# Performance work log

Hardware: AMD Instinct MI355X
Metric: run time of the kernel (lower is better)

The kernel has to match this reference:

```python
import jax, jax.numpy as jnp
import numpy as np


def _lap(cost):
    """Jonker-Volgenant / e-maxx O(n^3) Hungarian (min-cost) on a square
    float64 cost matrix. Returns col index assigned to each row, matching
    scipy.optimize.linear_sum_assignment for square inputs.
    Inner column scan is vectorized with numpy.
    """
    n = cost.shape[0]
    INF = np.inf
    C = np.zeros((n + 1, n + 1), dtype=np.float64)
    C[1:, 1:] = cost  # 1-indexed
    u = np.zeros(n + 1)
    v = np.zeros(n + 1)
    p = np.zeros(n + 1, dtype=np.int64)    # p[j] = row matched to col j
    way = np.zeros(n + 1, dtype=np.int64)
    for i in range(1, n + 1):
        p[0] = i
        j0 = 0
        minv = np.full(n + 1, INF)
        used = np.zeros(n + 1, dtype=bool)
        while True:
            used[j0] = True
            i0 = p[j0]
            free = ~used
            free[0] = False
            cur = C[i0] - u[i0] - v
            upd = free & (cur < minv)
            minv = np.where(upd, cur, minv)
            way[upd] = j0
            mv = np.where(free, minv, INF)
            j1 = int(np.argmin(mv))
            delta = mv[j1]
            u[p[used]] += delta
            v[used] -= delta
            minv = np.where(free, minv - delta, minv)
            j0 = j1
            if p[j0] == 0:
                break
        # augment along alternating path
        while j0 != 0:
            j1 = way[j0]
            p[j0] = p[j1]
            j0 = j1
    col_for_row = np.zeros(n, dtype=np.int64)
    col_for_row[p[1:] - 1] = np.arange(n)
    return col_for_row


def _match(D_np):
    """Per-sample min-max normalize (detached) then Hungarian match."""
    B, N, _ = D_np.shape
    cols = np.zeros((B, N), dtype=np.int64)
    for b in range(B):
        Db = D_np[b]
        d_min = Db.min()
        d_range = Db.max() - d_min + 1e-8
        cols[b] = _lap((Db - d_min) / d_range)
    return cols


def setup_inputs() -> dict:
    key = jax.random.key(0)
    B, N = 32, 512
    D = jax.random.uniform(key, (B, N, N), dtype=jnp.float32)
    return {"D": D}


def reference(D):
    B, N, _ = D.shape
    # Matching indices are computed on detached, normalized costs (CPU, like
    # the original .cpu().numpy() round-trip).
    D_np = np.asarray(jax.device_get(D), dtype=np.float64)
    cols = jnp.asarray(_match(D_np))                      # [B, N]
    bi = jnp.arange(B)[:, None]
    ri = jnp.arange(N)[None, :]
    matched = D[bi, ri, cols]                             # [B, N], original D
    return matched.mean(axis=1).mean()
```

## Files before the change

kernel.cpp:

```cpp
#include <hip/hip_runtime.h>
#include <hip/hip_fp16.h>


#define NN 512
#define LPT 8
#define BIGF 1e30f
#define QCAP 2080
#define ARRCAP 1536
#define TOTAL_BLOCKS 256

typedef float v2f __attribute__((ext_vector_type(2)));
#define EL(a, s) ((a)[(s) >> 1][(s) & 1])

#define DPP_MINF(x, CTRL) do {                                                  \
    float _t = __int_as_float(__builtin_amdgcn_update_dpp(                      \
        __float_as_int(x), __float_as_int(x), CTRL, 0xf, 0xf, false));          \
    (x) = _t < (x) ? _t : (x);                                                  \
} while (0)

__device__ __forceinline__ float wave_min_f32(float x) {
    DPP_MINF(x, 0x111);
    DPP_MINF(x, 0x112);
    DPP_MINF(x, 0x114);
    DPP_MINF(x, 0x118);
    DPP_MINF(x, 0x142);
    DPP_MINF(x, 0x143);
    return __int_as_float(__builtin_amdgcn_readlane(__float_as_int(x), 63));
}

__device__ __forceinline__ void wavebar() { __builtin_amdgcn_wave_barrier(); }

__device__ __forceinline__ int sel8i(const int a[LPT], int slot) {
    int r = a[0];
    #pragma unroll
    for (int s = 1; s < LPT; ++s) r = (slot == s) ? a[s] : r;
    return r;
}
__device__ __forceinline__ float sel8fv(const v2f a[4], int slot) {
    float r = a[0][0];
    r = (slot == 1) ? a[0][1] : r;
    r = (slot == 2) ? a[1][0] : r;
    r = (slot == 3) ? a[1][1] : r;
    r = (slot == 4) ? a[2][0] : r;
    r = (slot == 5) ? a[2][1] : r;
    r = (slot == 6) ? a[3][0] : r;
    r = (slot == 7) ? a[3][1] : r;
    return r;
}
__device__ __forceinline__ void argmin8v(const v2f e2[4], float& bv, int& bs) {
    const float e0 = e2[0][0], e1 = e2[0][1], e2_ = e2[1][0], e3 = e2[1][1];
    const float e4 = e2[2][0], e5 = e2[2][1], e6 = e2[3][0], e7 = e2[3][1];
    float v01 = e1 < e0 ? e1 : e0;   int s01 = e1 < e0 ? 1 : 0;
    float v23 = e3 < e2_ ? e3 : e2_; int s23 = e3 < e2_ ? 3 : 2;
    float v45 = e5 < e4 ? e5 : e4;   int s45 = e5 < e4 ? 5 : 4;
    float v67 = e7 < e6 ? e7 : e6;   int s67 = e7 < e6 ? 7 : 6;
    float v03 = v23 < v01 ? v23 : v01; int s03 = v23 < v01 ? s23 : s01;
    float v47 = v67 < v45 ? v67 : v45; int s47 = v67 < v45 ? s67 : s45;
    bv = v47 < v03 ? v47 : v03;        bs = v47 < v03 ? s47 : s03;
}

__global__ void zero_kernel(int* __restrict__ done) {
    if (threadIdx.x == 0) *done = 0;
}

template <bool F16>
__global__ __launch_bounds__(64)
void hungarian_kernel(const float* __restrict__ D, const __half* __restrict__ Hm,
                      double* __restrict__ bsum, int* __restrict__ done, int B) {
    const int b    = blockIdx.x;
    const int lane = threadIdx.x;

    if (b >= B) {
        const unsigned long long t0 = __builtin_amdgcn_s_memrealtime();
        float x = 1.0f + (float)lane * 1e-6f;
        while (true) {
            #pragma unroll
            for (int k = 0; k < 512; ++k) x = __builtin_fmaf(x, 1.0000001f, 1e-9f);
            if (__hip_atomic_load(done, __ATOMIC_RELAXED, __HIP_MEMORY_SCOPE_AGENT) >= B)
                break;
            if (__builtin_amdgcn_s_memrealtime() - t0 > 1200000ull)
                break;
        }
        if (x == -1.0f) bsum[B] = (double)x;
        return;
    }

    const float*  __restrict__ Db = D + (size_t)b * NN * NN;
    const __half* __restrict__ Hb = F16 ? (Hm + (size_t)b * NN * NN) : (const __half*)nullptr;

    __shared__ __align__(16) int xrowc[NN];
    __shared__ __align__(16) int q[QCAP];

    for (int k = lane; k < NN; k += 64) xrowc[k] = 0;
    wavebar();

    const int col0 = lane * LPT;

    auto loadrow = [&](int r, v2f rv[4]) {
        if constexpr (F16) {
            const uint4 qv = *(const uint4*)(Hb + (size_t)(r - 1) * NN + col0);
            __half2 h0 = *(__half2*)&qv.x, h1 = *(__half2*)&qv.y,
                    h2 = *(__half2*)&qv.z, h3 = *(__half2*)&qv.w;
            float2 f0 = __half22float2(h0), f1 = __half22float2(h1),
                   f2 = __half22float2(h2), f3 = __half22float2(h3);
            v2f t0 = {f0.x, f0.y}, t1 = {f1.x, f1.y}, t2 = {f2.x, f2.y}, t3 = {f3.x, f3.y};
            rv[0] = t0; rv[1] = t1; rv[2] = t2; rv[3] = t3;
        } else {
            const float4* rp = (const float4*)(Db + (size_t)(r - 1) * NN + col0);
            const float4 a = rp[0], c = rp[1];
            v2f t0 = {a.x, a.y}, t1 = {a.z, a.w}, t2 = {c.x, c.y}, t3 = {c.z, c.w};
            rv[0] = t0; rv[1] = t1; rv[2] = t2; rv[3] = t3;
        }
    };
    auto loadsc = [&](int r, int j) -> float {
        if constexpr (F16) return __half2float(Hb[(size_t)(r - 1) * NN + (j - 1)]);
        else               return Db[(size_t)(r - 1) * NN + (j - 1)];
    };

    v2f   vv[4];
    int   preg[LPT];
    int   xr[LPT];

    auto build_queue = [&]() -> int {
        int cnt = 0;
        #pragma unroll
        for (int s = 0; s < LPT; ++s) cnt += (xr[s] == 0) ? 1 : 0;
        int pre = cnt;
        #pragma unroll
        for (int d = 1; d < 64; d <<= 1) {
            const int t = __shfl_up(pre, d, 64);
            if (lane >= d) pre += t;
        }
        const int total = __builtin_amdgcn_readlane(pre, 63);
        int ofs = pre - cnt;
        #pragma unroll
        for (int s = 0; s < LPT; ++s)
            if (xr[s] == 0) { q[ofs] = col0 + s + 1; ++ofs; }
        wavebar();
        return total;
    };

    {
        float cmin[LPT]; int cidx[LPT];
        #pragma unroll
        for (int s = 0; s < LPT; ++s) { cmin[s] = BIGF; cidx[s] = 0; }
        #pragma unroll 4
        for (int r = 1; r <= NN; ++r) {
            v2f rvx[4]; loadrow(r, rvx);
            #pragma unroll
            for (int s = 0; s < LPT; ++s) {
                const float x = EL(rvx, s);
                const bool c = x < cmin[s];
                cidx[s] = c ? r : cidx[s];
                cmin[s] = c ? x : cmin[s];
            }
        }
        #pragma unroll
        for (int s = 0; s < LPT; ++s) EL(vv, s) = cmin[s];
        #pragma unroll
        for (int s = 0; s < LPT; ++s) atomicMax(&xrowc[cidx[s] - 1], col0 + s + 1);
        wavebar();
        #pragma unroll
        for (int s = 0; s < LPT; ++s)
            preg[s] = (xrowc[cidx[s] - 1] == col0 + s + 1) ? cidx[s] : 0;
        const int4 x0 = *(const int4*)&xrowc[col0];
        const int4 x1 = *(const int4*)&xrowc[col0 + 4];
        xr[0]=x0.x; xr[1]=x0.y; xr[2]=x0.z; xr[3]=x0.w;
        xr[4]=x1.x; xr[5]=x1.y; xr[6]=x1.z; xr[7]=x1.w;
    }
    wavebar();

    {
        auto readjx = [&](int i) -> int {
            return __builtin_amdgcn_readlane(sel8i(xr, (i - 1) & 7), (i - 1) >> 3);
        };
        int jxN = readjx(1);
        v2f rvN[4];
        if (jxN) loadrow(1, rvN);
        for (int i = 1; i <= NN; ++i) {
            const int jx = jxN;
            v2f rcur[4];
            #pragma unroll
            for (int k = 0; k < 4; ++k) rcur[k] = rvN[k];
            jxN = (i < NN) ? readjx(i + 1) : 0;
            if (jxN) loadrow(i + 1, rvN);
            if (jx == 0) continue;
            const int  ow = (jx - 1) >> 3, sl = (jx - 1) & 7;
            const bool am = (lane == ow);
            v2f d2[4];
            #pragma unroll
            for (int k = 0; k < 4; ++k) d2[k] = rcur[k] - vv[k];
            float lm = BIGF;
            #pragma unroll
            for (int s = 0; s < LPT; ++s) {
                const float t = (am && s == sl) ? BIGF : EL(d2, s);
                lm = t < lm ? t : lm;
            }
            const float mu = wave_min_f32(lm);
            #pragma unroll
            for (int s = 0; s < LPT; ++s)
                if (am && s == sl) EL(vv, s) = EL(rcur, s) - mu;
        }
    }

    {
        int tail = build_queue();
        int head = 0, processed = 0;
        int iCur = 0;
        v2f rvC[4];
        if (tail > 0) { iCur = q[0]; loadrow(iCur, rvC); }
        while (head < tail && processed < ARRCAP) {
            const int i = iCur; ++head; ++processed;
            v2f rvA[4];
            #pragma unroll
            for (int k = 0; k < 4; ++k) rvA[k] = rvC[k];
            int iNxt = (head < tail) ? q[head] : 0;
            if (iNxt) loadrow(iNxt, rvC);

            v2f cur[4];
            #pragma unroll
            for (int k = 0; k < 4; ++k) cur[k] = rvA[k] - vv[k];
            float b1; int bs1; argmin8v(cur, b1, bs1);
            const int i1c = sel8i(preg, bs1);
            const float u1 = wave_min_f32(b1);
            const unsigned long long m1 = __ballot(b1 == u1);
            const int owner = __ffsll(m1) - 1;
            const int j1    = __builtin_amdgcn_readlane(col0 + bs1 + 1, owner);
            const int i1    = __builtin_amdgcn_readlane(i1c, owner);
            const bool am   = (lane == owner);
            #pragma unroll
            for (int s = 0; s < LPT; ++s)
                if (am && s == bs1) EL(cur, s) = BIGF;
            float b2 = BIGF;
            #pragma unroll
            for (int s = 0; s < LPT; ++s) { const float t = EL(cur, s); b2 = t < b2 ? t : b2; }
            const float u2 = wave_min_f32(b2);
            const bool steal  = (u1 < u2);
            const bool assign = (i1 == 0) || (steal && (tail < QCAP - 1));
            if (assign) {
                #pragma unroll
                for (int s = 0; s < LPT; ++s) {
                    if (am && s == bs1) {
                        if (steal) EL(vv, s) -= (u2 - u1);
                        preg[s] = i;
                    }
                }
                if (lane == 0) {
                    xrowc[i - 1] = j1;
                    if (i1) { xrowc[i1 - 1] = 0; q[tail] = i1; }
                }
                if (i1) {
                    if (!iNxt) { iNxt = i1; loadrow(iNxt, rvC); }
                    ++tail;
                }
            }
            iCur = iNxt;
            wavebar();
        }
    }
    wavebar();

    {
        const int4 x0 = *(const int4*)&xrowc[col0];
        const int4 x1 = *(const int4*)&xrowc[col0 + 4];
        xr[0]=x0.x; xr[1]=x0.y; xr[2]=x0.z; xr[3]=x0.w;
        xr[4]=x1.x; xr[5]=x1.y; xr[6]=x1.z; xr[7]=x1.w;
    }
    const int nfree = build_queue();

    int rootNext = (nfree > 0) ? q[0] : 0;
    v2f rv[4];
    if (rootNext) loadrow(rootNext, rv);
    for (int fi = 0; fi < nfree; ++fi) {
        const int rootI = rootNext;
        rootNext = (fi + 1 < nfree) ? q[fi + 1] : 0;

        v2f minv2[4], blk2[4], w2[4];
        int wayreg[LPT];
        #pragma unroll
        for (int k = 0; k < 4; ++k) {
            v2f big = {BIGF, BIGF}, zero = {0.0f, 0.0f};
            minv2[k] = big; blk2[k] = zero;
        }
        #pragma unroll
        for (int s = 0; s < LPT; ++s) wayreg[s] = 0;
        float uu = 0.0f;
        int   j0 = 0;

        #pragma unroll
        for (int k = 0; k < 4; ++k) w2[k] = rv[k] - vv[k];

        int j1 = 0; float dmin = 0.0f;
        while (true) {
            const v2f uu2 = {uu, uu};
            v2f e2[4];
            #pragma unroll
            for (int k = 0; k < 4; ++k) {
                const v2f c2 = (w2[k] - uu2) + blk2[k];
                const float c0 = c2[0], c1 = c2[1];
                const bool u0 = c0 < minv2[k][0];
                const bool u1 = c1 < minv2[k][1];
                wayreg[2*k]   = u0 ? j0 : wayreg[2*k];
                wayreg[2*k+1] = u1 ? j0 : wayreg[2*k+1];
                v2f m = minv2[k];
                m[0] = u0 ? c0 : m[0];
                m[1] = u1 ? c1 : m[1];
                minv2[k] = m;
                e2[k] = m + blk2[k];
            }
            float bv; int bs; argmin8v(e2, bv, bs);
            const int   i0c = sel8i(preg, bs);
            const float vjc = sel8fv(vv, bs);
            dmin = wave_min_f32(bv);
            const unsigned long long mk = __ballot(bv == dmin);
            const int owner = __ffsll(mk) - 1;
            j1 = __builtin_amdgcn_readlane(col0 + bs + 1, owner);
            const int i0n = __builtin_amdgcn_readlane(i0c, owner);
            if (i0n == 0) break;

            const float csc = loadsc(i0n, j1);
            loadrow(i0n, rv);
            const float vj1 = __int_as_float(__builtin_amdgcn_readlane(
                __float_as_int(vjc), owner));
            const bool am = (lane == owner);
            #pragma unroll
            for (int s = 0; s < LPT; ++s)
                if (am && s == bs) EL(blk2, s) = BIGF;

            uu = csc - vj1 - dmin;
            #pragma unroll
            for (int k = 0; k < 4; ++k) w2[k] = rv[k] - vv[k];
            j0 = j1;
        }
        const float dfinal = dmin;
        j0 = j1;

        if (rootNext) loadrow(rootNext, rv);

        #pragma unroll
        for (int s = 0; s < LPT; ++s)
            if (EL(blk2, s) == BIGF) EL(vv, s) += EL(minv2, s) - dfinal;

        int jj = j0;
        while (jj != 0) {
            const int sl = (jj - 1) & 7, ln = (jj - 1) >> 3;
            const int jp = __builtin_amdgcn_readlane(sel8i(wayreg, sl), ln);
            int nr;
            if (jp != 0) {
                const int sp = (jp - 1) & 7, lp = (jp - 1) >> 3;
                nr = __builtin_amdgcn_readlane(sel8i(preg, sp), lp);
            } else {
                nr = rootI;
            }
            #pragma unroll
            for (int s = 0; s < LPT; ++s)
                if (lane == ln && s == sl) preg[s] = nr;
            jj = jp;
        }
    }

    double acc = 0.0;
    #pragma unroll
    for (int s = 0; s < LPT; ++s) {
        const int r = preg[s];
        acc += (double)Db[(size_t)(r - 1) * NN + (col0 + s)];
    }
    #pragma unroll
    for (int m = 1; m < 64; m <<= 1) acc += __shfl_xor(acc, m, 64);
    if (lane == 0) {
        bsum[b] = acc;
        __threadfence();
        atomicAdd(done, 1);
    }
}

__global__ void finalize_kernel(const double* __restrict__ bsum, float* __restrict__ out, int B) {
    if (threadIdx.x == 0 && blockIdx.x == 0) {
        double acc = 0.0;
        for (int b = 0; b < B; ++b) acc += bsum[b] / (double)NN;
        out[0] = (float)(acc / (double)B);
    }
}

extern "C" void kernel_launch(void* const* d_in, const int* in_sizes, int n_in,
                              void* d_out, int out_size, void* d_ws, size_t ws_size,
                              hipStream_t stream) {
    (void)n_in; (void)out_size; (void)ws_size;
    const float* D    = (const float*)d_in[0];
    float*       out  = (float*)d_out;
    int*         done = (int*)d_ws;
    double*      bsum = (double*)((char*)d_ws + 64);

    const int B = in_sizes[0] / (NN * NN);

    zero_kernel<<<1, 64, 0, stream>>>(done);
    hungarian_kernel<false><<<dim3(TOTAL_BLOCKS), dim3(64), 0, stream>>>(D, nullptr, bsum, done, B);
    finalize_kernel<<<1, 64, 0, stream>>>(bsum, out, B);
}
```

Measured before the change: 2.493 ms.

## Speculatively prefetch next Dijkstra row using argmin over existing minv before scan

Restructures the inner shortest-augmenting-path loop so that, after each step, the wave computes the argmin over the current minv (excluding used columns). It then issues the row and scalar load for that candidate column one iteration early. When a wave ballot shows no newly relaxed column beats that speculative minimum, the prefetched row is used directly, hiding global-load latency behind the relaxation work. This costs an extra wave-wide reduction per step plus a second row buffer in registers, and wastes loads when the speculation misses. The unused F16 template path is also removed.

```diff
diff --git a/kernel.cpp b/kernel.cpp
--- a/kernel.cpp
+++ b/kernel.cpp
@@ -63,9 +63,8 @@
     if (threadIdx.x == 0) *done = 0;
 }
 
-template <bool F16>
 __global__ __launch_bounds__(64)
-void hungarian_kernel(const float* __restrict__ D, const __half* __restrict__ Hm,
+void hungarian_kernel(const float* __restrict__ D,
                       double* __restrict__ bsum, int* __restrict__ done, int B) {
     const int b    = blockIdx.x;
     const int lane = threadIdx.x;
@@ -85,8 +84,7 @@
         return;
     }
 
-    const float*  __restrict__ Db = D + (size_t)b * NN * NN;
-    const __half* __restrict__ Hb = F16 ? (Hm + (size_t)b * NN * NN) : (const __half*)nullptr;
+    const float* __restrict__ Db = D + (size_t)b * NN * NN;
 
     __shared__ __align__(16) int xrowc[NN];
     __shared__ __align__(16) int q[QCAP];
@@ -97,24 +95,13 @@
     const int col0 = lane * LPT;
 
     auto loadrow = [&](int r, v2f rv[4]) {
-        if constexpr (F16) {
-            const uint4 qv = *(const uint4*)(Hb + (size_t)(r - 1) * NN + col0);
-            __half2 h0 = *(__half2*)&qv.x, h1 = *(__half2*)&qv.y,
-                    h2 = *(__half2*)&qv.z, h3 = *(__half2*)&qv.w;
-            float2 f0 = __half22float2(h0), f1 = __half22float2(h1),
-                   f2 = __half22float2(h2), f3 = __half22float2(h3);
-            v2f t0 = {f0.x, f0.y}, t1 = {f1.x, f1.y}, t2 = {f2.x, f2.y}, t3 = {f3.x, f3.y};
-            rv[0] = t0; rv[1] = t1; rv[2] = t2; rv[3] = t3;
-        } else {
-            const float4* rp = (const float4*)(Db + (size_t)(r - 1) * NN + col0);
-            const float4 a = rp[0], c = rp[1];
-            v2f t0 = {a.x, a.y}, t1 = {a.z, a.w}, t2 = {c.x, c.y}, t3 = {c.z, c.w};
-            rv[0] = t0; rv[1] = t1; rv[2] = t2; rv[3] = t3;
-        }
+        const float4* rp = (const float4*)(Db + (size_t)(r - 1) * NN + col0);
+        const float4 a = rp[0], c = rp[1];
+        v2f t0 = {a.x, a.y}, t1 = {a.z, a.w}, t2 = {c.x, c.y}, t3 = {c.z, c.w};
+        rv[0] = t0; rv[1] = t1; rv[2] = t2; rv[3] = t3;
     };
     auto loadsc = [&](int r, int j) -> float {
-        if constexpr (F16) return __half2float(Hb[(size_t)(r - 1) * NN + (j - 1)]);
-        else               return Db[(size_t)(r - 1) * NN + (j - 1)];
+        return Db[(size_t)(r - 1) * NN + (j - 1)];
     };
 
     v2f   vv[4];
@@ -269,13 +256,14 @@
     const int nfree = build_queue();
 
     int rootNext = (nfree > 0) ? q[0] : 0;
-    v2f rv[4];
-    if (rootNext) loadrow(rootNext, rv);
+    v2f rvR[4], rvP[4];
+    float cscR = 0.0f, cscP = 0.0f;
+    if (rootNext) loadrow(rootNext, rvR);
     for (int fi = 0; fi < nfree; ++fi) {
         const int rootI = rootNext;
         rootNext = (fi + 1 < nfree) ? q[fi + 1] : 0;
 
-        v2f minv2[4], blk2[4], w2[4];
+        v2f minv2[4], blk2[4];
         int wayreg[LPT];
         #pragma unroll
         for (int k = 0; k < 4; ++k) {
@@ -284,58 +272,105 @@
         }
         #pragma unroll
         for (int s = 0; s < LPT; ++s) wayreg[s] = 0;
-        float uu = 0.0f;
+
         int   j0 = 0;
-
-        #pragma unroll
-        for (int k = 0; k < 4; ++k) w2[k] = rv[k] - vv[k];
+        float Me = BIGF; int j1E = 0, i0E = 0; float vjE = 0.0f;
+        float vjW = 0.0f, dminPrev = 0.0f;
+        bool  useSpec = false;
+        cscR = 0.0f;
 
         int j1 = 0; float dmin = 0.0f;
         while (true) {
+            v2f rvU[4]; float cscU;
+            if (useSpec) {
+                #pragma unroll
+                for (int k = 0; k < 4; ++k) rvU[k] = rvP[k];
+                cscU = cscP;
+            } else {
+                #pragma unroll
+                for (int k = 0; k < 4; ++k) rvU[k] = rvR[k];
+                cscU = cscR;
+            }
+            if (i0E != 0) {
+                cscP = loadsc(i0E, j1E);
+                loadrow(i0E, rvP);
+            }
+            const float uu = cscU - vjW - dminPrev;
             const v2f uu2 = {uu, uu};
-            v2f e2[4];
+            v2f c2[4], cs[4];
             #pragma unroll
             for (int k = 0; k < 4; ++k) {
-                const v2f c2 = (w2[k] - uu2) + blk2[k];
-                const float c0 = c2[0], c1 = c2[1];
-                const bool u0 = c0 < minv2[k][0];
-                const bool u1 = c1 < minv2[k][1];
+                const v2f w2 = rvU[k] - vv[k];
+                c2[k] = (w2 - uu2) + blk2[k];
+                cs[k] = c2[k] + blk2[k];
+            }
+            float bv_c; int bs_c; argmin8v(cs, bv_c, bs_c);
+            const int   i0cC = sel8i(preg, bs_c);
+            const float vjcC = sel8fv(vv, bs_c);
+            #pragma unroll
+            for (int k = 0; k < 4; ++k) {
+                const bool u0 = c2[k][0] < minv2[k][0];
+                const bool u1 = c2[k][1] < minv2[k][1];
                 wayreg[2*k]   = u0 ? j0 : wayreg[2*k];
                 wayreg[2*k+1] = u1 ? j0 : wayreg[2*k+1];
                 v2f m = minv2[k];
-                m[0] = u0 ? c0 : m[0];
-                m[1] = u1 ? c1 : m[1];
+                m[0] = u0 ? c2[k][0] : m[0];
+                m[1] = u1 ? c2[k][1] : m[1];
                 minv2[k] = m;
-                e2[k] = m + blk2[k];
-            }
-            float bv; int bs; argmin8v(e2, bv, bs);
-            const int   i0c = sel8i(preg, bs);
-            const float vjc = sel8fv(vv, bs);
-            dmin = wave_min_f32(bv);
-            const unsigned long long mk = __ballot(bv == dmin);
-            const int owner = __ffsll(mk) - 1;
-            j1 = __builtin_amdgcn_readlane(col0 + bs + 1, owner);
-            const int i0n = __builtin_amdgcn_readlane(i0c, owner);
+            }
+            int i0n;
+            const unsigned long long tst = __ballot(bv_c <= Me);
+            if (tst == 0ull) {
+                j1 = j1E; i0n = i0E; vjW = vjE; dmin = Me;
+                useSpec = true;
+            } else {
+                const float Mc = wave_min_f32(bv_c);
+                const unsigned long long mkc = __ballot(bv_c == Mc);
+                const int ownerC = __ffsll(mkc) - 1;
+                const int j1C = __builtin_amdgcn_readlane(col0 + bs_c + 1, ownerC);
+                const int i0C = __builtin_amdgcn_readlane(i0cC, ownerC);
+                const float vjC = __int_as_float(__builtin_amdgcn_readlane(
+                    __float_as_int(vjcC), ownerC));
+                dmin = Mc;
+                if (Mc == Me && j1E < j1C) {
+                    j1 = j1E; i0n = i0E; vjW = vjE; useSpec = true;
+                } else {
+                    j1 = j1C; i0n = i0C; vjW = vjC; useSpec = false;
+                }
+            }
             if (i0n == 0) break;
-
-            const float csc = loadsc(i0n, j1);
-            loadrow(i0n, rv);
-            const float vj1 = __int_as_float(__builtin_amdgcn_readlane(
-                __float_as_int(vjc), owner));
-            const bool am = (lane == owner);
-            #pragma unroll
-            for (int s = 0; s < LPT; ++s)
-                if (am && s == bs) EL(blk2, s) = BIGF;
-
-            uu = csc - vj1 - dmin;
-            #pragma unroll
-            for (int k = 0; k < 4; ++k) w2[k] = rv[k] - vv[k];
-            j0 = j1;
+            if (!useSpec) {
+                cscR = loadsc(i0n, j1);
+                loadrow(i0n, rvR);
+            }
+            {
+                const int ow = (j1 - 1) >> 3, sl = (j1 - 1) & 7;
+                const bool am = (lane == ow);
+                #pragma unroll
+                for (int s = 0; s < LPT; ++s)
+                    if (am && s == sl) EL(blk2, s) = BIGF;
+            }
+            j0 = j1; dminPrev = dmin;
+            {
+                v2f es[4];
+                #pragma unroll
+                for (int k = 0; k < 4; ++k) es[k] = minv2[k] + blk2[k];
+                float bv_e; int bs_e; argmin8v(es, bv_e, bs_e);
+                const int   i0cE = sel8i(preg, bs_e);
+                const float vjcE = sel8fv(vv, bs_e);
+                Me = wave_min_f32(bv_e);
+                const unsigned long long mke = __ballot(bv_e == Me);
+                const int ownerE = __ffsll(mke) - 1;
+                j1E = __builtin_amdgcn_readlane(col0 + bs_e + 1, ownerE);
+                i0E = __builtin_amdgcn_readlane(i0cE, ownerE);
+                vjE = __int_as_float(__builtin_amdgcn_readlane(
+                    __float_as_int(vjcE), ownerE));
+            }
         }
         const float dfinal = dmin;
         j0 = j1;
 
-        if (rootNext) loadrow(rootNext, rv);
+        if (rootNext) { cscR = 0.0f; loadrow(rootNext, rvR); }
 
         #pragma unroll
         for (int s = 0; s < LPT; ++s)
@@ -394,6 +429,6 @@
     const int B = in_sizes[0] / (NN * NN);
 
     zero_kernel<<<1, 64, 0, stream>>>(done);
-    hungarian_kernel<false><<<dim3(TOTAL_BLOCKS), dim3(64), 0, stream>>>(D, nullptr, bsum, done, B);
+    hungarian_kernel<<<dim3(TOTAL_BLOCKS), dim3(64), 0, stream>>>(D, bsum, done, B);
     finalize_kernel<<<1, 64, 0, stream>>>(bsum, out, B);
 }
```

New measurement: 3.302 ms. +32.5%, slower.
